# Optimization experiments

Hardware: AMD Instinct MI355X
Metric: run time of the kernel (lower is better)

## Reference

```python
import jax, jax.numpy as jnp
import numpy as np

B, MBITS, P = 4096, 64, 64
BLK = P // 8          # 8: block size for crop-robust pattern
FREQ = P // 4         # 16: low-res frequency pattern size
KS, SIGMA = 5, 1.0


def _interp_matrix(n_in, n_out):
    # 1D bilinear interpolation matrix with align_corners=True semantics
    pos = jnp.arange(n_out, dtype=jnp.float32) * (n_in - 1) / (n_out - 1)
    lo = jnp.floor(pos).astype(jnp.int32)
    hi = jnp.minimum(lo + 1, n_in - 1)
    w = pos - lo.astype(jnp.float32)
    rows = jnp.arange(n_out)
    M = jnp.zeros((n_out, n_in), jnp.float32)
    M = M.at[rows, lo].add(1.0 - w).at[rows, hi].add(w)
    return M


def _gaussian_kernel(ks, sigma):
    c = jnp.arange(ks, dtype=jnp.float32) - ks // 2
    g = jnp.exp(-c**2 / (2.0 * sigma**2))
    g = g / g.sum()
    k2 = jnp.outer(g, g)
    return k2 / k2.sum()


def setup_inputs() -> dict:
    key = jax.random.key(0)
    ks = jax.random.split(key, 8)

    def lin(k, fan_in, fan_out):
        lim = 1.0 / np.sqrt(fan_in)
        return jax.random.uniform(k, (fan_in, fan_out), jnp.float32, -lim, lim)

    return {
        'message': jax.random.uniform(ks[0], (B, MBITS), jnp.float32),
        'sW1': lin(ks[1], MBITS, 256), 'sb1': jnp.zeros((256,), jnp.float32),
        'sW2': lin(ks[2], 256, 512),   'sb2': jnp.zeros((512,), jnp.float32),
        'sW3': lin(ks[3], 512, P * P), 'sb3': jnp.zeros((P * P,), jnp.float32),
        'fW1': lin(ks[4], MBITS, 128), 'fb1': jnp.zeros((128,), jnp.float32),
        'fW2': lin(ks[5], 128, FREQ * FREQ), 'fb2': jnp.zeros((FREQ * FREQ,), jnp.float32),
    }


def reference(message, sW1, sb1, sW2, sb2, sW3, sb3, fW1, fb1, fW2, fb2):
    b = message.shape[0]
    # --- spatial pattern: MLP -> tanh -> [B,1,P,P]
    h = jax.nn.relu(message @ sW1 + sb1)
    h = jax.nn.relu(h @ sW2 + sb2)
    spatial = jnp.tanh(h @ sW3 + sb3).reshape(b, 1, P, P)

    # --- frequency pattern: MLP -> tanh -> [B,1,16,16] -> bilinear upsample to PxP
    f = jax.nn.relu(message @ fW1 + fb1)
    freq_lo = jnp.tanh(f @ fW2 + fb2).reshape(b, FREQ, FREQ)
    M = _interp_matrix(FREQ, P)  # [P, FREQ]
    freq = jnp.einsum('ph,bhw,qw->bpq', M, freq_lo, M)[:, None]  # [B,1,P,P]

    # --- block pattern: bit i -> 8x8 block (row-major over an 8x8 grid)
    blocks = message.reshape(b, 8, 8)  # [B, rows, cols] of bits
    block = jnp.repeat(jnp.repeat(blocks, BLK, axis=1), BLK, axis=2)[:, None]  # [B,1,P,P]

    rgb = jnp.concatenate([spatial, freq, block], axis=1)  # [B,3,P,P]

    # --- depthwise 5x5 Gaussian smoothing, groups=3
    k2 = _gaussian_kernel(KS, SIGMA)
    kernel = jnp.broadcast_to(k2, (3, 1, KS, KS))
    out = jax.lax.conv_general_dilated(
        rgb, kernel, window_strides=(1, 1), padding=[(KS // 2, KS // 2)] * 2,
        dimension_numbers=('NCHW', 'OIHW', 'NCHW'), feature_group_count=3)
    return out
```

## Files before the change

### kernel.cpp

```cpp
#include <hip/hip_runtime.h>
#include <math.h>

#define BATCH 4096

typedef __attribute__((ext_vector_type(8))) short short8;
typedef __attribute__((ext_vector_type(4))) float f32x4;

__device__ __forceinline__ unsigned short f2bf(float f) {
  unsigned int u = __float_as_uint(f);
  u += 0x7FFF + ((u >> 16) & 1);
  return (unsigned short)(u >> 16);
}

__device__ __forceinline__ float bf2f(unsigned short s) {
  return __uint_as_float(((unsigned int)s) << 16);
}

__device__ __forceinline__ float fast_tanh(float x) {
  const float e = __expf(2.0f * x);
  const float r = __builtin_amdgcn_rcpf(e + 1.0f);
  return fmaf(-2.0f, r, 1.0f);
}

#define GLL16(g, l)                                                    \
  __builtin_amdgcn_global_load_lds(                                    \
      (const __attribute__((address_space(1))) unsigned int*)(g),      \
      (__attribute__((address_space(3))) unsigned int*)(l), 16, 0, 0)

__global__ __launch_bounds__(256) void setup_kernel(
    const float* __restrict__ sW1, const float* __restrict__ sW2,
    const float* __restrict__ sW3, const float* __restrict__ msg,
    const float* __restrict__ fW1, const float* __restrict__ fb1,
    const float* __restrict__ fW2, const float* __restrict__ fb2,
    unsigned short* __restrict__ w1T, unsigned short* __restrict__ w2T,
    unsigned short* __restrict__ w3T, unsigned short* __restrict__ msgb,
    float* __restrict__ fl) {
  const int blk = blockIdx.x;
  const int t = threadIdx.x;

  __shared__ float ms[16 * 64];
  __shared__ float f1[16][128];
  __shared__ float tl[32][33];

  if (blk < 256) {
    const int row0 = blk * 16;
    *reinterpret_cast<float4*>(&ms[t * 4]) =
        *reinterpret_cast<const float4*>(&msg[(size_t)row0 * 64 + t * 4]);
    __syncthreads();
    {
      const int n = t & 127;
      const int rb = (t >> 7) * 8;
      float acc[8] = {};
      for (int k = 0; k < 64; ++k) {
        const float wv = fW1[k * 128 + n];
#pragma unroll
        for (int r = 0; r < 8; ++r) acc[r] += ms[(rb + r) * 64 + k] * wv;
      }
      const float bv = fb1[n];
#pragma unroll
      for (int r = 0; r < 8; ++r) f1[rb + r][n] = fmaxf(acc[r] + bv, 0.0f);
    }
    __syncthreads();
    {
      float acc[16] = {};
      for (int k = 0; k < 128; ++k) {
        const float wv = fW2[k * 256 + t];
#pragma unroll
        for (int r = 0; r < 16; ++r) acc[r] += f1[r][k] * wv;
      }
      const float bv = fb2[t];
#pragma unroll
      for (int r = 0; r < 16; ++r)
        fl[(size_t)(row0 + r) * 256 + t] = fast_tanh(acc[r] + bv);
    }
    return;
  }

  const int b = blk - 256;
  if (b >= 2192) {
    const int i0 = (b - 2192) * 2048 + t * 8;
    const float4 v0 = *reinterpret_cast<const float4*>(&msg[i0]);
    const float4 v1 = *reinterpret_cast<const float4*>(&msg[i0 + 4]);
    short8 o;
    o[0] = (short)f2bf(v0.x); o[1] = (short)f2bf(v0.y);
    o[2] = (short)f2bf(v0.z); o[3] = (short)f2bf(v0.w);
    o[4] = (short)f2bf(v1.x); o[5] = (short)f2bf(v1.y);
    o[6] = (short)f2bf(v1.z); o[7] = (short)f2bf(v1.w);
    *reinterpret_cast<short8*>(&msgb[i0]) = o;
    return;
  }

  const float* src;
  unsigned short* dst;
  int K, N, lgtN, tile;
  if (b < 16) {
    src = sW1; dst = w1T; K = 64; N = 256; lgtN = 3; tile = b;
  } else if (b < 144) {
    src = sW2; dst = w2T; K = 256; N = 512; lgtN = 4; tile = b - 16;
  } else {
    src = sW3; dst = w3T; K = 512; N = 4096; lgtN = 7; tile = b - 144;
  }
  const int ty = tile >> lgtN;
  const int tx = tile & ((1 << lgtN) - 1);

  {
    const int r = t >> 3, c4 = (t & 7) * 4;
    const float4 v =
        *reinterpret_cast<const float4*>(&src[(size_t)(ty * 32 + r) * N + tx * 32 + c4]);
    tl[r][c4 + 0] = v.x; tl[r][c4 + 1] = v.y;
    tl[r][c4 + 2] = v.z; tl[r][c4 + 3] = v.w;
  }
  __syncthreads();
  {
    const int nl = t >> 3, k4 = (t & 7) * 4;
    unsigned short o[4];
#pragma unroll
    for (int i = 0; i < 4; ++i) o[i] = f2bf(tl[k4 + i][nl]);
    *reinterpret_cast<ushort4*>(&dst[(size_t)(tx * 32 + nl) * K + ty * 32 + k4]) =
        *reinterpret_cast<const ushort4*>(o);
  }
}

template <int ACT, int OBF16, int KDIM, int NWG>
__global__ __launch_bounds__(256) void gemm_mfma(
    const unsigned short* __restrict__ A, const unsigned short* __restrict__ BT,
    const float* __restrict__ bias, void* __restrict__ Cv, int ldc) {
  __shared__ __align__(16) unsigned short As[2][128 * 32];
  __shared__ __align__(16) unsigned short Bs[2][128 * 32];

  const int t = threadIdx.x;
  const int lane = t & 63;
  const int w = t >> 6;

  const int orig = blockIdx.y * 32 + blockIdx.x;
  const int swz = (orig & 7) * (NWG >> 3) + (orig >> 3);
  const int bm = (swz & 31) * 128;
  const int bn = (swz >> 5) * 128;

  const int r0 = w * 32 + (lane >> 2);
  const int r1 = r0 + 16;
  const int c0 = (lane & 3) ^ ((r0 >> 1) & 3);
  const int c1 = (lane & 3) ^ ((r1 >> 1) & 3);

  const unsigned short* gA0 = A + (size_t)(bm + r0) * KDIM + c0 * 8;
  const unsigned short* gA1 = A + (size_t)(bm + r1) * KDIM + c1 * 8;
  const unsigned short* gB0 = BT + (size_t)(bn + r0) * KDIM + c0 * 8;
  const unsigned short* gB1 = BT + (size_t)(bn + r1) * KDIM + c1 * 8;

  const int lofs0 = (w * 2 + 0) * 512;
  const int lofs1 = (w * 2 + 1) * 512;

  const int wm = (w >> 1) * 64;
  const int wn = (w & 1) * 64;
  const int lr = lane & 15;
  const int lc = lane >> 4;
  int aoff[4], boff[4];
#pragma unroll
  for (int i = 0; i < 4; ++i) {
    const int arow = wm + i * 16 + lr;
    aoff[i] = arow * 32 + (lc ^ ((arow >> 1) & 3)) * 8;
    const int brow = wn + i * 16 + lr;
    boff[i] = brow * 32 + (lc ^ ((brow >> 1) & 3)) * 8;
  }

  f32x4 acc[4][4];
  const f32x4 z = {0.f, 0.f, 0.f, 0.f};
#pragma unroll
  for (int i = 0; i < 4; ++i)
#pragma unroll
    for (int j = 0; j < 4; ++j) acc[i][j] = z;

  constexpr int NT = KDIM / 32;

  GLL16(gA0, &As[0][lofs0]);
  GLL16(gA1, &As[0][lofs1]);
  GLL16(gB0, &Bs[0][lofs0]);
  GLL16(gB1, &Bs[0][lofs1]);
  gA0 += 32; gA1 += 32; gB0 += 32; gB1 += 32;
  __syncthreads();

  int cur = 0;
#pragma unroll 1
  for (int kt = 0; kt < NT; ++kt) {
    if (kt + 1 < NT) {
      const int nxt = cur ^ 1;
      GLL16(gA0, &As[nxt][lofs0]);
      GLL16(gA1, &As[nxt][lofs1]);
      GLL16(gB0, &Bs[nxt][lofs0]);
      GLL16(gB1, &Bs[nxt][lofs1]);
      gA0 += 32; gA1 += 32; gB0 += 32; gB1 += 32;
    }

    short8 a[4], b[4];
#pragma unroll
    for (int i = 0; i < 4; ++i)
      a[i] = *reinterpret_cast<const short8*>(&As[cur][aoff[i]]);
#pragma unroll
    for (int j = 0; j < 4; ++j)
      b[j] = *reinterpret_cast<const short8*>(&Bs[cur][boff[j]]);

#pragma unroll
    for (int i = 0; i < 4; ++i)
#pragma unroll
      for (int j = 0; j < 4; ++j)
        acc[i][j] =
            __builtin_amdgcn_mfma_f32_16x16x32_bf16(a[i], b[j], acc[i][j], 0, 0, 0);

    __syncthreads();
    cur ^= 1;
  }

  const int base_row = bm + wm + (lc << 2);
  const int base_col = bn + wn + lr;
#pragma unroll
  for (int i = 0; i < 4; ++i) {
#pragma unroll
    for (int j = 0; j < 4; ++j) {
      const int n = base_col + j * 16;
      const float bv = bias[n];
#pragma unroll
      for (int r = 0; r < 4; ++r) {
        const int m = base_row + i * 16 + r;
        float v = acc[i][j][r] + bv;
        v = (ACT == 0) ? fmaxf(v, 0.0f) : fast_tanh(v);
        if (OBF16)
          ((unsigned short*)Cv)[(size_t)m * ldc + n] = f2bf(v);
        else
          ((float*)Cv)[(size_t)m * ldc + n] = v;
      }
    }
  }
}

__global__ __launch_bounds__(256) void finalize_kernel(
    const float* __restrict__ msg, const float* __restrict__ fl_in,
    const unsigned short* __restrict__ spatial, float* __restrict__ out) {
  const int b = blockIdx.x;
  const int c = blockIdx.y;
  const int t = threadIdx.x;

  __shared__ float chan[4096];
  __shared__ float tmp[4096];
  __shared__ float fl[256];
  __shared__ float msgs[64];
  __shared__ int lo_tab[64];
  __shared__ float w_tab[64];

  const float g0 = 0.054488684549644346f;
  const float g1 = 0.24420134200323332f;
  const float g2 = 0.4026199468907953f;
  const float g[5] = {g0, g1, g2, g1, g0};

  if (c != 0) {
    if (t < 64) {
      msgs[t] = msg[(size_t)b * 64 + t];
      const float pos = (float)t * (15.0f / 63.0f);
      int lo = (int)floorf(pos);
      if (lo > 15) lo = 15;
      lo_tab[t] = lo;
      w_tab[t] = pos - (float)lo;
    }
    fl[t] = fl_in[(size_t)b * 256 + t];
  }
  __syncthreads();

  if (c == 0) {
    const short8* sp = reinterpret_cast<const short8*>(spatial + (size_t)b * 4096);
    for (int v = t; v < 512; v += 256) {
      const short8 s = sp[v];
#pragma unroll
      for (int j = 0; j < 8; ++j) chan[v * 8 + j] = bf2f((unsigned short)s[j]);
    }
  } else if (c == 1) {
    for (int i = t; i < 4096; i += 256) {
      const int p = i >> 6, q = i & 63;
      const int lp = lo_tab[p], lq = lo_tab[q];
      const int hp = lp < 15 ? lp + 1 : 15;
      const int hq = lq < 15 ? lq + 1 : 15;
      const float wp = w_tab[p], wq = w_tab[q];
      const float v00 = fl[lp * 16 + lq], v01 = fl[lp * 16 + hq];
      const float v10 = fl[hp * 16 + lq], v11 = fl[hp * 16 + hq];
      chan[i] = (1.0f - wp) * ((1.0f - wq) * v00 + wq * v01) +
                wp * ((1.0f - wq) * v10 + wq * v11);
    }
  } else {
    for (int i = t; i < 4096; i += 256) {
      const int p = i >> 6, q = i & 63;
      chan[i] = msgs[((p >> 3) << 3) + (q >> 3)];
    }
  }
  __syncthreads();

  for (int i = t; i < 4096; i += 256) {
    const int p = i >> 6, q = i & 63;
    float s = 0.0f;
#pragma unroll
    for (int d = -2; d <= 2; ++d) {
      const int qq = q + d;
      if (qq >= 0 && qq < 64) s += g[d + 2] * chan[p * 64 + qq];
    }
    tmp[i] = s;
  }
  __syncthreads();

  float4* dst = reinterpret_cast<float4*>(out + (size_t)b * 12288 + (size_t)c * 4096);
  for (int i = t; i < 1024; i += 256) {
    const int p = i >> 4;
    const int q4 = (i & 15) * 4;
    float s0 = 0.f, s1 = 0.f, s2 = 0.f, s3 = 0.f;
#pragma unroll
    for (int d = -2; d <= 2; ++d) {
      const int pp = p + d;
      if (pp >= 0 && pp < 64) {
        const float gg = g[d + 2];
        const int base = pp * 64 + q4;
        s0 += gg * tmp[base + 0];
        s1 += gg * tmp[base + 1];
        s2 += gg * tmp[base + 2];
        s3 += gg * tmp[base + 3];
      }
    }
    float4 v;
    v.x = s0; v.y = s1; v.z = s2; v.w = s3;
    dst[i] = v;
  }
}

extern "C" void kernel_launch(void* const* d_in, const int* in_sizes, int n_in,
                              void* d_out, int out_size, void* d_ws,
                              size_t ws_size, hipStream_t stream) {
  const float* msg = (const float*)d_in[0];
  const float* sW1 = (const float*)d_in[1];
  const float* sb1 = (const float*)d_in[2];
  const float* sW2 = (const float*)d_in[3];
  const float* sb2 = (const float*)d_in[4];
  const float* sW3 = (const float*)d_in[5];
  const float* sb3 = (const float*)d_in[6];
  const float* fW1 = (const float*)d_in[7];
  const float* fb1 = (const float*)d_in[8];
  const float* fW2 = (const float*)d_in[9];
  const float* fb2 = (const float*)d_in[10];

  float* out = (float*)d_out;
  char* wsb = (char*)d_ws;

  unsigned short* msgb = (unsigned short*)(wsb);
  unsigned short* w1T  = (unsigned short*)(wsb + (1 << 19));
  unsigned short* w2T  = (unsigned short*)(wsb + (1 << 20));
  unsigned short* w3T  = (unsigned short*)(wsb + (2 << 20));
  unsigned short* h1   = (unsigned short*)(wsb + (8 << 20));
  unsigned short* h2   = (unsigned short*)(wsb + (12 << 20));
  unsigned short* spat = (unsigned short*)(wsb + (16 << 20));
  float* fl            = (float*)(wsb + (48 << 20));

  const dim3 blk(256);

  setup_kernel<<<dim3(2576), blk, 0, stream>>>(sW1, sW2, sW3, msg, fW1, fb1,
                                               fW2, fb2, w1T, w2T, w3T, msgb, fl);

  gemm_mfma<0, 1, 64, 64><<<dim3(32, 2), blk, 0, stream>>>(msgb, w1T, sb1, h1, 256);
  gemm_mfma<0, 1, 256, 128><<<dim3(32, 4), blk, 0, stream>>>(h1, w2T, sb2, h2, 512);
  gemm_mfma<1, 1, 512, 1024><<<dim3(32, 32), blk, 0, stream>>>(h2, w3T, sb3, spat, 4096);

  finalize_kernel<<<dim3(BATCH, 3), blk, 0, stream>>>(msg, fl, spat, out);
}
```

Measured before the change: 337.9 us.

## Use explicit vmcnt waits in GEMM loop and vectorize smoothing kernel LDS access

In the GEMM main loop, the full __syncthreads is replaced with an explicit s_waitcnt vmcnt that waits only for the current tile's global-to-LDS loads, so the next tile's prefetch can stay in flight across the barrier, followed by raw s_barrier calls. The smoothing kernel now uses float4 LDS reads and writes for the bf16 unpack, the block-pattern fill, and both separable Gaussian passes, which cuts the number of LDS instructions. The horizontal pass uses named coefficients g0..g2, whose definitions are not visible here, and relies on a hand-tuned vmcnt count that must match the number of loads issued.

```diff
diff --git a/kernel.cpp b/kernel.cpp
--- a/kernel.cpp
+++ b/kernel.cpp
@@ -177,7 +177,6 @@
   GLL16(gB0, &Bs[0][lofs0]);
   GLL16(gB1, &Bs[0][lofs1]);
   gA0 += 32; gA1 += 32; gB0 += 32; gB1 += 32;
-  __syncthreads();
 
   int cur = 0;
 #pragma unroll 1
@@ -189,7 +188,12 @@
       GLL16(gB0, &Bs[nxt][lofs0]);
       GLL16(gB1, &Bs[nxt][lofs1]);
       gA0 += 32; gA1 += 32; gB0 += 32; gB1 += 32;
-    }
+      asm volatile("s_waitcnt vmcnt(4)" ::: "memory");
+    } else {
+      asm volatile("s_waitcnt vmcnt(0)" ::: "memory");
+    }
+    __builtin_amdgcn_sched_barrier(0);
+    __builtin_amdgcn_s_barrier();
 
     short8 a[4], b[4];
 #pragma unroll
@@ -206,7 +210,7 @@
         acc[i][j] =
             __builtin_amdgcn_mfma_f32_16x16x32_bf16(a[i], b[j], acc[i][j], 0, 0, 0);
 
-    __syncthreads();
+    __builtin_amdgcn_s_barrier();
     cur ^= 1;
   }
 
@@ -268,8 +272,13 @@
     const short8* sp = reinterpret_cast<const short8*>(spatial + (size_t)b * 4096);
     for (int v = t; v < 512; v += 256) {
       const short8 s = sp[v];
-#pragma unroll
-      for (int j = 0; j < 8; ++j) chan[v * 8 + j] = bf2f((unsigned short)s[j]);
+      float4 lo4, hi4;
+      lo4.x = bf2f((unsigned short)s[0]); lo4.y = bf2f((unsigned short)s[1]);
+      lo4.z = bf2f((unsigned short)s[2]); lo4.w = bf2f((unsigned short)s[3]);
+      hi4.x = bf2f((unsigned short)s[4]); hi4.y = bf2f((unsigned short)s[5]);
+      hi4.z = bf2f((unsigned short)s[6]); hi4.w = bf2f((unsigned short)s[7]);
+      *reinterpret_cast<float4*>(&chan[v * 8]) = lo4;
+      *reinterpret_cast<float4*>(&chan[v * 8 + 4]) = hi4;
     }
   } else if (c == 1) {
     for (int i = t; i < 4096; i += 256) {
@@ -284,45 +293,46 @@
                 wp * ((1.0f - wq) * v10 + wq * v11);
     }
   } else {
-    for (int i = t; i < 4096; i += 256) {
-      const int p = i >> 6, q = i & 63;
-      chan[i] = msgs[((p >> 3) << 3) + (q >> 3)];
+    for (int i = t; i < 1024; i += 256) {
+      const int p = i >> 4, q4 = (i & 15) * 4;
+      const float v = msgs[((p >> 3) << 3) + (q4 >> 3)];
+      float4 sv; sv.x = v; sv.y = v; sv.z = v; sv.w = v;
+      *reinterpret_cast<float4*>(&chan[p * 64 + q4]) = sv;
     }
   }
   __syncthreads();
 
-  for (int i = t; i < 4096; i += 256) {
-    const int p = i >> 6, q = i & 63;
-    float s = 0.0f;
-#pragma unroll
-    for (int d = -2; d <= 2; ++d) {
-      const int qq = q + d;
-      if (qq >= 0 && qq < 64) s += g[d + 2] * chan[p * 64 + qq];
-    }
-    tmp[i] = s;
+  for (int i = t; i < 1024; i += 256) {
+    const int p = i >> 4, q4 = (i & 15) * 4;
+    const float* row = &chan[p * 64];
+    const float4 C = *reinterpret_cast<const float4*>(&row[q4]);
+    float4 L = {0.f, 0.f, 0.f, 0.f}, R = {0.f, 0.f, 0.f, 0.f};
+    if (q4 > 0) L = *reinterpret_cast<const float4*>(&row[q4 - 4]);
+    if (q4 < 60) R = *reinterpret_cast<const float4*>(&row[q4 + 4]);
+    float4 o;
+    o.x = g0 * L.z + g1 * L.w + g2 * C.x + g1 * C.y + g0 * C.z;
+    o.y = g0 * L.w + g1 * C.x + g2 * C.y + g1 * C.z + g0 * C.w;
+    o.z = g0 * C.x + g1 * C.y + g2 * C.z + g1 * C.w + g0 * R.x;
+    o.w = g0 * C.y + g1 * C.z + g2 * C.w + g1 * R.x + g0 * R.y;
+    *reinterpret_cast<float4*>(&tmp[p * 64 + q4]) = o;
   }
   __syncthreads();
 
   float4* dst = reinterpret_cast<float4*>(out + (size_t)b * 12288 + (size_t)c * 4096);
   for (int i = t; i < 1024; i += 256) {
-    const int p = i >> 4;
-    const int q4 = (i & 15) * 4;
-    float s0 = 0.f, s1 = 0.f, s2 = 0.f, s3 = 0.f;
+    const int p = i >> 4, q4 = (i & 15) * 4;
+    float4 acc = {0.f, 0.f, 0.f, 0.f};
 #pragma unroll
     for (int d = -2; d <= 2; ++d) {
       const int pp = p + d;
       if (pp >= 0 && pp < 64) {
         const float gg = g[d + 2];
-        const int base = pp * 64 + q4;
-        s0 += gg * tmp[base + 0];
-        s1 += gg * tmp[base + 1];
-        s2 += gg * tmp[base + 2];
-        s3 += gg * tmp[base + 3];
+        const float4 tv = *reinterpret_cast<const float4*>(&tmp[pp * 64 + q4]);
+        acc.x += gg * tv.x; acc.y += gg * tv.y;
+        acc.z += gg * tv.z; acc.w += gg * tv.w;
       }
     }
-    float4 v;
-    v.x = s0; v.y = s1; v.z = s2; v.w = s3;
-    dst[i] = v;
+    dst[i] = acc;
   }
 }
 
```

Result: faster. 308.4 us (-8.8%).
